# Kernel tuning notes

Measured on AMD Instinct MI355X. Metric: run time of the kernel, lower is better.

## Reference

```python
import jax, jax.numpy as jnp
import numpy as np

B = 65536
H = 50          # hidden_size
L = 6           # num_layers
IN = 3          # input_size
T = 3           # seq_len


def setup_inputs() -> dict:
    key = jax.random.key(0)
    ks = jax.random.split(key, 10)
    s = 0.1  # weight init scale
    return {
        "x":     jax.random.normal(ks[0], (B, IN, T), dtype=jnp.float32),
        "h0":    jax.random.normal(ks[1], (L, B, H), dtype=jnp.float32),
        "c0":    jax.random.normal(ks[2], (L, B, H), dtype=jnp.float32),
        "w_ih0": jax.random.normal(ks[3], (4 * H, IN), dtype=jnp.float32) * s,
        "w_ih":  jax.random.normal(ks[4], (L - 1, 4 * H, H), dtype=jnp.float32) * s,
        "w_hh":  jax.random.normal(ks[5], (L, 4 * H, H), dtype=jnp.float32) * s,
        "b_ih":  jax.random.normal(ks[6], (L, 4 * H), dtype=jnp.float32) * s,
        "b_hh":  jax.random.normal(ks[7], (L, 4 * H), dtype=jnp.float32) * s,
        "fc_w":  jax.random.normal(ks[8], (1, H), dtype=jnp.float32) * s,
        "fc_b":  jax.random.normal(ks[9], (1,), dtype=jnp.float32) * s,
    }


def _lstm_layer(x_seq, h, c, w_ih, w_hh, b):
    """x_seq: [T, B, in]; returns all hidden states [T, B, H].
    PyTorch gate order: i, f, g, o."""
    def step(carry, x_t):
        h, c = carry
        gates = x_t @ w_ih.T + h @ w_hh.T + b  # [B, 4H]
        i, f, g, o = jnp.split(gates, 4, axis=-1)
        i = jax.nn.sigmoid(i)
        f = jax.nn.sigmoid(f)
        g = jnp.tanh(g)
        o = jax.nn.sigmoid(o)
        c = f * c + i * g
        h = o * jnp.tanh(c)
        return (h, c), h

    _, ys = jax.lax.scan(step, (h, c), x_seq)
    return ys


def reference(x, h0, c0, w_ih0, w_ih, w_hh, b_ih, b_hh, fc_w, fc_b):
    # original forward: input.permute(0, 2, 1) -> [B, T, IN], batch_first LSTM
    seq = jnp.transpose(x, (2, 0, 1))  # [T, B, IN] (time-major for scan)
    b = b_ih + b_hh                    # combined bias per layer [L, 4H]
    ys = _lstm_layer(seq, h0[0], c0[0], w_ih0, w_hh[0], b[0])
    for l in range(1, L):
        ys = _lstm_layer(ys, h0[l], c0[l], w_ih[l - 1], w_hh[l], b[l])
    # dropout(0.2) is identity in eval mode; take last timestep then fc
    last = ys[-1]                      # [B, H]
    return last @ fc_w.T + fc_b        # [B, 1]
```

## Files before the change

### kernel.cpp

```cpp
#include <hip/hip_runtime.h>


namespace {

constexpr int H  = 50;
constexpr int L  = 6;
constexpr int T  = 3;
constexpr int IN = 3;
constexpr int M  = 64;
constexpr int BLK = 512;
constexpr int ROWS = 72;

using half8  = __attribute__((ext_vector_type(8))) _Float16;
using half2v = __attribute__((ext_vector_type(2))) _Float16;
using f32x4  = __attribute__((ext_vector_type(4))) float;

__device__ __forceinline__ float rcp_(float x) { return __builtin_amdgcn_rcpf(x); }
__device__ __forceinline__ float ex2(float x)  { return __builtin_amdgcn_exp2f(x); }

__global__ void wprep(const float* __restrict__ w_ih0, const float* __restrict__ w_ihL,
                      const float* __restrict__ w_hh,  const float* __restrict__ b_ih,
                      const float* __restrict__ b_hh,  _Float16* __restrict__ wbuf) {
  int t = blockIdx.x * 256 + threadIdx.x;
  if (t >= 384 * 64) return;
  int lam = t & 63, f = t >> 6;
  int nt = f & 15, s = (f >> 4) & 3, l = f >> 6;
  int n = nt * 16 + (lam & 15);
  int j = n >> 2, gate = n & 3, row = gate * 50 + j;
  float scale = (gate == 2) ? 2.8853900817779268f : 1.4426950408889634f;
  _Float16 o8[8];
#pragma unroll
  for (int jj = 0; jj < 8; ++jj) {
    int k = s * 32 + (lam >> 4) * 8 + jj;
    float v = 0.f;
    if (j < H) {
      if (s < 2) {
        int ksz = (l == 0) ? IN : H;
        if (k < ksz) v = (l == 0) ? w_ih0[row * IN + k]
                                  : w_ihL[((size_t)(l - 1) * 200 + row) * H + k];
      } else {
        int kh = k - 64;
        if (kh < H)        v = w_hh[((size_t)l * 200 + row) * H + kh];
        else if (kh == 63) v = b_ih[l * 200 + row] + b_hh[l * 200 + row];
      }
    }
    o8[jj] = (_Float16)(v * scale);
  }
  ((half8*)wbuf)[t] = *(half8*)o8;
}

__global__ __launch_bounds__(BLK, 4)
void lstm_mfma(const float* __restrict__ x,   const float* __restrict__ h0,
               const float* __restrict__ c0,  const float* __restrict__ fc_w,
               const float* __restrict__ fc_b, const _Float16* __restrict__ wbuf,
               float* __restrict__ out, int B) {
  const int tid = threadIdx.x;
  const int lam = tid & 63;
  const int q   = lam >> 4;
  const int lm  = lam & 15;
  const int bbase = blockIdx.x * M;
  const int ng  = __builtin_amdgcn_readfirstlane(tid >> 6);
  const int ntp = __builtin_amdgcn_readfirstlane((ng + blockIdx.x) & 7);
  const int ntg0 = 2 * ntp, ntg1 = 2 * ntp + 1;
  const bool live0 = (ntg0 <= 12);
  const bool live1 = (ntg1 <= 12);

  __shared__ __align__(16) _Float16 ys[2][T][M][ROWS];

  if (tid < T * M) {
    const int t = tid >> 6, m = tid & 63;
    const float* xs = x + (size_t)(bbase + m) * (IN * T) + t;
    _Float16* row = &ys[0][t][m][0];
    half2v p0; p0[0] = (_Float16)xs[0]; p0[1] = (_Float16)xs[3];
    half2v p1; p1[0] = (_Float16)xs[6]; p1[1] = (_Float16)0.f;
    *(half2v*)(row)     = p0;
    *(half2v*)(row + 2) = p1;
#pragma unroll
    for (int z = 0; z < 7; ++z)
      *(unsigned long long*)(row + 4 + 4 * z) = 0ull;
  }
  if (tid < 2 * T * M) {
    _Float16* row = &ys[0][0][0][0] + (size_t)tid * ROWS;
#pragma unroll
    for (int z = 0; z < 6; ++z)
      *(unsigned int*)(row + 50 + 2 * z) = 0u;
    half2v pb; pb[0] = (_Float16)0.f; pb[1] = (_Float16)1.f;
    *(half2v*)(row + 62) = pb;
  }
  __syncthreads();

  float cc[2][4];
  f32x4 xa[2][4];
  half8 W[2][4];
  const f32x4 z4 = {0.f, 0.f, 0.f, 0.f};

  for (int l = 0; l < L; ++l) {
    const int sb = l & 1, db = sb ^ 1;
    _Float16 (*src)[M][ROWS] = ys[sb];
    _Float16 (*dst)[M][ROWS] = ys[db];

#pragma unroll
    for (int nt = 0; nt < 2; ++nt) {
      const int ntg = nt ? ntg1 : ntg0;
      const bool lv = nt ? live1 : live0;
      const int j = 4 * ntg + q;
#pragma unroll
      for (int mt = 0; mt < 4; ++mt)
        cc[nt][mt] = (lv && j < H)
            ? c0[((size_t)l * B + bbase + mt * 16 + lm) * H + j] : 0.f;
    }
#pragma unroll
    for (int nt = 0; nt < 2; ++nt) {
      const int ntg = nt ? ntg1 : ntg0;
      const bool lv = nt ? live1 : live0;
      if (lv)
#pragma unroll
        for (int s = 0; s < 4; ++s)
          W[nt][s] = ((const half8*)wbuf)[((l * 4 + s) * 16 + ntg) * 64 + lam];
    }

    if (live0) {
#pragma unroll
      for (int s = 0; s < 2; ++s) {
        if (s == 1 && l == 0) continue;
        half8 Xf[4];
#pragma unroll
        for (int mt = 0; mt < 4; ++mt)
          Xf[mt] = *(const half8*)(&src[0][mt * 16 + lm][s * 32 + q * 8]);
#pragma unroll
        for (int mt = 0; mt < 4; ++mt)
          xa[0][mt] = __builtin_amdgcn_mfma_f32_16x16x32_f16(
              W[0][s], Xf[mt], s == 0 ? z4 : xa[0][mt], 0, 0, 0);
        if (live1)
#pragma unroll
          for (int mt = 0; mt < 4; ++mt)
            xa[1][mt] = __builtin_amdgcn_mfma_f32_16x16x32_f16(
                W[1][s], Xf[mt], s == 0 ? z4 : xa[1][mt], 0, 0, 0);
      }
    }

    {
      const int mg = tid >> 3, kpl = tid & 7;
      const float* hp = h0 + ((size_t)l * B + bbase + mg) * H + 2 * kpl;
      _Float16* dp = &dst[T - 1][mg][2 * kpl];
#pragma unroll
      for (int it = 0; it < 4; ++it) {
        if (it < 3 || kpl == 0) {
          float2 v = *(const float2*)(hp + 16 * it);
          half2v pv; pv[0] = (_Float16)v.x; pv[1] = (_Float16)v.y;
          *(half2v*)(dp + 16 * it) = pv;
        }
      }
    }
    __syncthreads();

#pragma unroll
    for (int t = 0; t < T; ++t) {
      const int hsl = (t == 0) ? T - 1 : t - 1;
      if (live0) {
#pragma unroll
        for (int s = 0; s < 2; ++s) {
          half8 Xf[4];
#pragma unroll
          for (int mt = 0; mt < 4; ++mt)
            Xf[mt] = *(const half8*)(&dst[hsl][mt * 16 + lm][s * 32 + q * 8]);
#pragma unroll
          for (int mt = 0; mt < 4; ++mt)
            xa[0][mt] = __builtin_amdgcn_mfma_f32_16x16x32_f16(
                W[0][s + 2], Xf[mt], xa[0][mt], 0, 0, 0);
          if (live1)
#pragma unroll
            for (int mt = 0; mt < 4; ++mt)
              xa[1][mt] = __builtin_amdgcn_mfma_f32_16x16x32_f16(
                  W[1][s + 2], Xf[mt], xa[1][mt], 0, 0, 0);
        }

#pragma unroll
        for (int nt = 0; nt < 2; ++nt) {
          if (nt && !live1) continue;
          const int ntg = nt ? ntg1 : ntg0;
          const int j = 4 * ntg + q;
#pragma unroll
          for (int mt = 0; mt < 4; ++mt) {
            const float ig = rcp_(1.f + ex2(-xa[nt][mt][0]));
            const float fg = rcp_(1.f + ex2(-xa[nt][mt][1]));
            const float gg = 2.f * rcp_(1.f + ex2(-xa[nt][mt][2])) - 1.f;
            const float og = rcp_(1.f + ex2(-xa[nt][mt][3]));
            const float cv = fg * cc[nt][mt] + ig * gg;
            cc[nt][mt] = cv;
            const float tc = 2.f * rcp_(1.f + ex2(-2.8853900817779268f * cv)) - 1.f;
            const float hv = og * tc;
            if (j < H)
              dst[t][mt * 16 + lm][j] = (_Float16)hv;
          }
        }

        if (t < T - 1) {
#pragma unroll
          for (int s = 0; s < 2; ++s) {
            if (s == 1 && l == 0) continue;
            half8 Xf[4];
#pragma unroll
            for (int mt = 0; mt < 4; ++mt)
              Xf[mt] = *(const half8*)(&src[t + 1][mt * 16 + lm][s * 32 + q * 8]);
#pragma unroll
            for (int mt = 0; mt < 4; ++mt)
              xa[0][mt] = __builtin_amdgcn_mfma_f32_16x16x32_f16(
                  W[0][s], Xf[mt], s == 0 ? z4 : xa[0][mt], 0, 0, 0);
            if (live1)
#pragma unroll
              for (int mt = 0; mt < 4; ++mt)
                xa[1][mt] = __builtin_amdgcn_mfma_f32_16x16x32_f16(
                    W[1][s], Xf[mt], s == 0 ? z4 : xa[1][mt], 0, 0, 0);
          }
        }
      }
      __syncthreads();
    }
  }

  {
    int m = tid >> 3, strip = tid & 7;
    float part = 0.f;
#pragma unroll
    for (int jj = 0; jj < 7; ++jj) {
      int j = strip + 8 * jj;
      if (j < H) part += fc_w[j] * (float)ys[0][T - 1][m][j];
    }
    part += __shfl_xor(part, 4);
    part += __shfl_xor(part, 2);
    part += __shfl_xor(part, 1);
    if (strip == 0) out[bbase + m] = part + fc_b[0];
  }
}

}

extern "C" void kernel_launch(void* const* d_in, const int* in_sizes, int n_in,
                              void* d_out, int out_size, void* d_ws, size_t ws_size,
                              hipStream_t stream) {
  const float* x     = (const float*)d_in[0];
  const float* h0    = (const float*)d_in[1];
  const float* c0    = (const float*)d_in[2];
  const float* w_ih0 = (const float*)d_in[3];
  const float* w_ih  = (const float*)d_in[4];
  const float* w_hh  = (const float*)d_in[5];
  const float* b_ih  = (const float*)d_in[6];
  const float* b_hh  = (const float*)d_in[7];
  const float* fc_w  = (const float*)d_in[8];
  const float* fc_b  = (const float*)d_in[9];
  float* out         = (float*)d_out;

  const int B = in_sizes[0] / (IN * T);
  _Float16* wbuf = (_Float16*)d_ws;

  wprep<<<(384 * 64 + 255) / 256, 256, 0, stream>>>(w_ih0, w_ih, w_hh, b_ih, b_hh, wbuf);
  lstm_mfma<<<B / M, BLK, 0, stream>>>(x, h0, c0, fc_w, fc_b, wbuf, out, B);
}
```

Measured before the change: 269.6 us.

## Software-pipeline LSTM timestep: interleave MFMA, gate activations and next-step input projection

Restructures the per-timestep loop so it walks the four row tiles one at a time. For each tile it issues the recurrent MFMAs, then runs the gate activations and the next timestep's input-projection MFMAs for the previous tile. LDS operand loads are double-buffered in 2-slot register arrays instead of 4-wide fragment arrays. The aim is to overlap transcendental VALU work and LDS latency with matrix-core work and to lower peak register use. The cost is more complex code whose real benefit depends on how the compiler schedules it.

```diff
diff --git a/kernel.cpp b/kernel.cpp
--- a/kernel.cpp
+++ b/kernel.cpp
@@ -154,69 +154,77 @@
     }
     __syncthreads();
 
+#define LD_H(s, mt) (*(const half8*)(&dst[hsl][(mt) * 16 + lm][(s) * 32 + q * 8]))
+#define LD_X(s, mt) (*(const half8*)(&src[t + 1][(mt) * 16 + lm][(s) * 32 + q * 8]))
+#define ACT1(nt, mt) do {                                                      \
+    const int j_ = 4 * ((nt) ? ntg1 : ntg0) + q;                               \
+    const float ig = rcp_(1.f + ex2(-xa[nt][mt][0]));                          \
+    const float fg = rcp_(1.f + ex2(-xa[nt][mt][1]));                          \
+    const float gg = 2.f * rcp_(1.f + ex2(-xa[nt][mt][2])) - 1.f;              \
+    const float og = rcp_(1.f + ex2(-xa[nt][mt][3]));                          \
+    const float cv = fg * cc[nt][mt] + ig * gg;                                \
+    cc[nt][mt] = cv;                                                           \
+    const float tc = 2.f * rcp_(1.f + ex2(-2.8853900817779268f * cv)) - 1.f;   \
+    const float hv = og * tc;                                                  \
+    if (j_ < H) dst[t][(mt) * 16 + lm][j_] = (_Float16)hv;                     \
+  } while (0)
+#define XM1(nt, mt) do {                                                       \
+    xa[nt][mt] = __builtin_amdgcn_mfma_f32_16x16x32_f16(                       \
+        W[nt][0], Xn[0][(mt) & 1], z4, 0, 0, 0);                               \
+    if (l > 0)                                                                 \
+      xa[nt][mt] = __builtin_amdgcn_mfma_f32_16x16x32_f16(                     \
+          W[nt][1], Xn[1][(mt) & 1], xa[nt][mt], 0, 0, 0);                     \
+  } while (0)
+#define STEP_TAIL(mt) do {                                                     \
+    ACT1(0, mt);                                                               \
+    if (live1) ACT1(1, mt);                                                    \
+    if (pre) { XM1(0, mt); if (live1) XM1(1, mt); }                            \
+  } while (0)
+
 #pragma unroll
     for (int t = 0; t < T; ++t) {
       const int hsl = (t == 0) ? T - 1 : t - 1;
       if (live0) {
-#pragma unroll
-        for (int s = 0; s < 2; ++s) {
-          half8 Xf[4];
-#pragma unroll
-          for (int mt = 0; mt < 4; ++mt)
-            Xf[mt] = *(const half8*)(&dst[hsl][mt * 16 + lm][s * 32 + q * 8]);
-#pragma unroll
-          for (int mt = 0; mt < 4; ++mt)
-            xa[0][mt] = __builtin_amdgcn_mfma_f32_16x16x32_f16(
-                W[0][s + 2], Xf[mt], xa[0][mt], 0, 0, 0);
-          if (live1)
-#pragma unroll
-            for (int mt = 0; mt < 4; ++mt)
-              xa[1][mt] = __builtin_amdgcn_mfma_f32_16x16x32_f16(
-                  W[1][s + 2], Xf[mt], xa[1][mt], 0, 0, 0);
+        const bool pre = (t < T - 1);
+        half8 Hf[2][2], Xn[2][2];
+        Hf[0][0] = LD_H(0, 0);
+        Hf[1][0] = LD_H(1, 0);
+        if (pre) {
+          Xn[0][0] = LD_X(0, 0);
+          if (l > 0) Xn[1][0] = LD_X(1, 0);
         }
-
-#pragma unroll
-        for (int nt = 0; nt < 2; ++nt) {
-          if (nt && !live1) continue;
-          const int ntg = nt ? ntg1 : ntg0;
-          const int j = 4 * ntg + q;
-#pragma unroll
-          for (int mt = 0; mt < 4; ++mt) {
-            const float ig = rcp_(1.f + ex2(-xa[nt][mt][0]));
-            const float fg = rcp_(1.f + ex2(-xa[nt][mt][1]));
-            const float gg = 2.f * rcp_(1.f + ex2(-xa[nt][mt][2])) - 1.f;
-            const float og = rcp_(1.f + ex2(-xa[nt][mt][3]));
-            const float cv = fg * cc[nt][mt] + ig * gg;
-            cc[nt][mt] = cv;
-            const float tc = 2.f * rcp_(1.f + ex2(-2.8853900817779268f * cv)) - 1.f;
-            const float hv = og * tc;
-            if (j < H)
-              dst[t][mt * 16 + lm][j] = (_Float16)hv;
+#pragma unroll
+        for (int mt = 0; mt < 4; ++mt) {
+          const int cur = mt & 1, nxt = cur ^ 1;
+          if (mt < 3) {
+            Hf[0][nxt] = LD_H(0, mt + 1);
+            Hf[1][nxt] = LD_H(1, mt + 1);
+          }
+          xa[0][mt] = __builtin_amdgcn_mfma_f32_16x16x32_f16(
+              W[0][2], Hf[0][cur], xa[0][mt], 0, 0, 0);
+          xa[0][mt] = __builtin_amdgcn_mfma_f32_16x16x32_f16(
+              W[0][3], Hf[1][cur], xa[0][mt], 0, 0, 0);
+          if (live1) {
+            xa[1][mt] = __builtin_amdgcn_mfma_f32_16x16x32_f16(
+                W[1][2], Hf[0][cur], xa[1][mt], 0, 0, 0);
+            xa[1][mt] = __builtin_amdgcn_mfma_f32_16x16x32_f16(
+                W[1][3], Hf[1][cur], xa[1][mt], 0, 0, 0);
+          }
+          if (mt > 0) STEP_TAIL(mt - 1);
+          if (mt < 3 && pre) {
+            Xn[0][nxt] = LD_X(0, mt + 1);
+            if (l > 0) Xn[1][nxt] = LD_X(1, mt + 1);
           }
         }
-
-        if (t < T - 1) {
-#pragma unroll
-          for (int s = 0; s < 2; ++s) {
-            if (s == 1 && l == 0) continue;
-            half8 Xf[4];
-#pragma unroll
-            for (int mt = 0; mt < 4; ++mt)
-              Xf[mt] = *(const half8*)(&src[t + 1][mt * 16 + lm][s * 32 + q * 8]);
-#pragma unroll
-            for (int mt = 0; mt < 4; ++mt)
-              xa[0][mt] = __builtin_amdgcn_mfma_f32_16x16x32_f16(
-                  W[0][s], Xf[mt], s == 0 ? z4 : xa[0][mt], 0, 0, 0);
-            if (live1)
-#pragma unroll
-              for (int mt = 0; mt < 4; ++mt)
-                xa[1][mt] = __builtin_amdgcn_mfma_f32_16x16x32_f16(
-                    W[1][s], Xf[mt], s == 0 ? z4 : xa[1][mt], 0, 0, 0);
-          }
-        }
+        STEP_TAIL(3);
       }
       __syncthreads();
     }
+#undef LD_H
+#undef LD_X
+#undef ACT1
+#undef XM1
+#undef STEP_TAIL
   }
 
   {
```

Result: no change. 271.6 us (+0.8%).

## Use 16 waves per block with one gate tile each and a rotating 5-slot LDS ring

Applied to the files above, without the earlier changes.

Doubles the block size from 8 to 16 waves so each wave owns a single 16-column gate tile instead of two, halving the per-wave MFMA and activation work and the register footprint. The layer double buffer of six timestep slots becomes a rotating ring of five slots, where each layer's outputs overwrite consumed inputs. This cuts LDS per block and lets more blocks fit per CU. The trade-off is that 3 of 16 waves are idle, and barriers now synchronise twice as many waves.

```diff
diff --git a/kernel.cpp b/kernel.cpp
--- a/kernel.cpp
+++ b/kernel.cpp
@@ -8,8 +8,9 @@
 constexpr int T  = 3;
 constexpr int IN = 3;
 constexpr int M  = 64;
-constexpr int BLK = 512;
+constexpr int BLK = 1024;
 constexpr int ROWS = 72;
+constexpr int NSLOT = 5;
 
 using half8  = __attribute__((ext_vector_type(8))) _Float16;
 using half2v = __attribute__((ext_vector_type(2))) _Float16;
@@ -49,7 +50,7 @@
   ((half8*)wbuf)[t] = *(half8*)o8;
 }
 
-__global__ __launch_bounds__(BLK, 4)
+__global__ __launch_bounds__(BLK, 8)
 void lstm_mfma(const float* __restrict__ x,   const float* __restrict__ h0,
                const float* __restrict__ c0,  const float* __restrict__ fc_w,
                const float* __restrict__ fc_b, const _Float16* __restrict__ wbuf,
@@ -59,18 +60,25 @@
   const int q   = lam >> 4;
   const int lm  = lam & 15;
   const int bbase = blockIdx.x * M;
-  const int ng  = __builtin_amdgcn_readfirstlane(tid >> 6);
-  const int ntp = __builtin_amdgcn_readfirstlane((ng + blockIdx.x) & 7);
-  const int ntg0 = 2 * ntp, ntg1 = 2 * ntp + 1;
-  const bool live0 = (ntg0 <= 12);
-  const bool live1 = (ntg1 <= 12);
-
-  __shared__ __align__(16) _Float16 ys[2][T][M][ROWS];
-
+  const int w   = __builtin_amdgcn_readfirstlane(tid >> 6);
+  const int ntg = __builtin_amdgcn_readfirstlane((w + blockIdx.x) & 15);
+  const bool live = (ntg <= 12);
+  const int j = 4 * ntg + q;
+
+  __shared__ __align__(16) _Float16 ys[NSLOT][M][ROWS];
+
+  if (tid < NSLOT * M) {
+    _Float16* row = &ys[0][0][0] + (size_t)tid * ROWS;
+#pragma unroll
+    for (int z = 0; z < 6; ++z)
+      *(unsigned int*)(row + 50 + 2 * z) = 0u;
+    half2v pb; pb[0] = (_Float16)0.f; pb[1] = (_Float16)1.f;
+    *(half2v*)(row + 62) = pb;
+  }
   if (tid < T * M) {
     const int t = tid >> 6, m = tid & 63;
     const float* xs = x + (size_t)(bbase + m) * (IN * T) + t;
-    _Float16* row = &ys[0][t][m][0];
+    _Float16* row = &ys[2 + t][m][0];
     half2v p0; p0[0] = (_Float16)xs[0]; p0[1] = (_Float16)xs[3];
     half2v p1; p1[0] = (_Float16)xs[6]; p1[1] = (_Float16)0.f;
     *(half2v*)(row)     = p0;
@@ -79,153 +87,109 @@
     for (int z = 0; z < 7; ++z)
       *(unsigned long long*)(row + 4 + 4 * z) = 0ull;
   }
-  if (tid < 2 * T * M) {
-    _Float16* row = &ys[0][0][0][0] + (size_t)tid * ROWS;
-#pragma unroll
-    for (int z = 0; z < 6; ++z)
-      *(unsigned int*)(row + 50 + 2 * z) = 0u;
-    half2v pb; pb[0] = (_Float16)0.f; pb[1] = (_Float16)1.f;
-    *(half2v*)(row + 62) = pb;
-  }
   __syncthreads();
 
-  float cc[2][4];
-  f32x4 xa[2][4];
-  half8 W[2][4];
+  float cc[4];
+  f32x4 xa[4];
+  half8 W4[4];
   const f32x4 z4 = {0.f, 0.f, 0.f, 0.f};
+  int b = 0;
 
   for (int l = 0; l < L; ++l) {
-    const int sb = l & 1, db = sb ^ 1;
-    _Float16 (*src)[M][ROWS] = ys[sb];
-    _Float16 (*dst)[M][ROWS] = ys[db];
-
-#pragma unroll
-    for (int nt = 0; nt < 2; ++nt) {
-      const int ntg = nt ? ntg1 : ntg0;
-      const bool lv = nt ? live1 : live0;
-      const int j = 4 * ntg + q;
+    const int sh0 = b;
+    int s1 = b + 1; if (s1 >= NSLOT) s1 -= NSLOT;
+    int s2 = b + 2; if (s2 >= NSLOT) s2 -= NSLOT;
+    int s3 = b + 3; if (s3 >= NSLOT) s3 -= NSLOT;
+    int s4 = b + 4; if (s4 >= NSLOT) s4 -= NSLOT;
+
+    if (live) {
 #pragma unroll
       for (int mt = 0; mt < 4; ++mt)
-        cc[nt][mt] = (lv && j < H)
+        cc[mt] = (j < H)
             ? c0[((size_t)l * B + bbase + mt * 16 + lm) * H + j] : 0.f;
-    }
-#pragma unroll
-    for (int nt = 0; nt < 2; ++nt) {
-      const int ntg = nt ? ntg1 : ntg0;
-      const bool lv = nt ? live1 : live0;
-      if (lv)
-#pragma unroll
-        for (int s = 0; s < 4; ++s)
-          W[nt][s] = ((const half8*)wbuf)[((l * 4 + s) * 16 + ntg) * 64 + lam];
-    }
-
-    if (live0) {
-#pragma unroll
-      for (int s = 0; s < 2; ++s) {
-        if (s == 1 && l == 0) continue;
-        half8 Xf[4];
-#pragma unroll
-        for (int mt = 0; mt < 4; ++mt)
-          Xf[mt] = *(const half8*)(&src[0][mt * 16 + lm][s * 32 + q * 8]);
-#pragma unroll
-        for (int mt = 0; mt < 4; ++mt)
-          xa[0][mt] = __builtin_amdgcn_mfma_f32_16x16x32_f16(
-              W[0][s], Xf[mt], s == 0 ? z4 : xa[0][mt], 0, 0, 0);
-        if (live1)
-#pragma unroll
-          for (int mt = 0; mt < 4; ++mt)
-            xa[1][mt] = __builtin_amdgcn_mfma_f32_16x16x32_f16(
-                W[1][s], Xf[mt], s == 0 ? z4 : xa[1][mt], 0, 0, 0);
-      }
-    }
-
+#pragma unroll
+      for (int s = 0; s < 4; ++s)
+        W4[s] = ((const half8*)wbuf)[((l * 4 + s) * 16 + ntg) * 64 + lam];
+#pragma unroll
+      for (int mt = 0; mt < 4; ++mt) {
+        half8 X0 = *(const half8*)(&ys[s2][mt * 16 + lm][q * 8]);
+        xa[mt] = __builtin_amdgcn_mfma_f32_16x16x32_f16(W4[0], X0, z4, 0, 0, 0);
+      }
+      if (l > 0) {
+#pragma unroll
+        for (int mt = 0; mt < 4; ++mt) {
+          half8 X1 = *(const half8*)(&ys[s2][mt * 16 + lm][32 + q * 8]);
+          xa[mt] = __builtin_amdgcn_mfma_f32_16x16x32_f16(W4[1], X1, xa[mt], 0, 0, 0);
+        }
+      }
+    }
     {
-      const int mg = tid >> 3, kpl = tid & 7;
+      const int mg = tid >> 4, kpl = tid & 15;
       const float* hp = h0 + ((size_t)l * B + bbase + mg) * H + 2 * kpl;
-      _Float16* dp = &dst[T - 1][mg][2 * kpl];
-#pragma unroll
-      for (int it = 0; it < 4; ++it) {
-        if (it < 3 || kpl == 0) {
-          float2 v = *(const float2*)(hp + 16 * it);
-          half2v pv; pv[0] = (_Float16)v.x; pv[1] = (_Float16)v.y;
-          *(half2v*)(dp + 16 * it) = pv;
+      _Float16* dp = &ys[sh0][mg][2 * kpl];
+      float2 v = *(const float2*)(hp);
+      half2v pv; pv[0] = (_Float16)v.x; pv[1] = (_Float16)v.y;
+      *(half2v*)dp = pv;
+      if (kpl < 9) {
+        float2 v2 = *(const float2*)(hp + 32);
+        half2v p2; p2[0] = (_Float16)v2.x; p2[1] = (_Float16)v2.y;
+        *(half2v*)(dp + 32) = p2;
+      }
+    }
+    __syncthreads();
+
+#pragma unroll
+    for (int t = 0; t < T; ++t) {
+      const int shs = (t == 0) ? sh0 : ((t == 1) ? s1 : s2);
+      const int sot = (t == 0) ? s1  : ((t == 1) ? s2 : s3);
+      const int sxt = (t == 0) ? s3  : s4;
+      if (live) {
+#pragma unroll
+        for (int s = 0; s < 2; ++s)
+#pragma unroll
+          for (int mt = 0; mt < 4; ++mt) {
+            half8 Hf = *(const half8*)(&ys[shs][mt * 16 + lm][s * 32 + q * 8]);
+            xa[mt] = __builtin_amdgcn_mfma_f32_16x16x32_f16(W4[2 + s], Hf, xa[mt], 0, 0, 0);
+          }
+#pragma unroll
+        for (int mt = 0; mt < 4; ++mt) {
+          const float ig = rcp_(1.f + ex2(-xa[mt][0]));
+          const float fg = rcp_(1.f + ex2(-xa[mt][1]));
+          const float gg = 2.f * rcp_(1.f + ex2(-xa[mt][2])) - 1.f;
+          const float og = rcp_(1.f + ex2(-xa[mt][3]));
+          const float cv = fg * cc[mt] + ig * gg;
+          cc[mt] = cv;
+          const float tc = 2.f * rcp_(1.f + ex2(-2.8853900817779268f * cv)) - 1.f;
+          if (j < H)
+            ys[sot][mt * 16 + lm][j] = (_Float16)(og * tc);
         }
-      }
-    }
-    __syncthreads();
-
-#pragma unroll
-    for (int t = 0; t < T; ++t) {
-      const int hsl = (t == 0) ? T - 1 : t - 1;
-      if (live0) {
-#pragma unroll
-        for (int s = 0; s < 2; ++s) {
-          half8 Xf[4];
-#pragma unroll
-          for (int mt = 0; mt < 4; ++mt)
-            Xf[mt] = *(const half8*)(&dst[hsl][mt * 16 + lm][s * 32 + q * 8]);
-#pragma unroll
-          for (int mt = 0; mt < 4; ++mt)
-            xa[0][mt] = __builtin_amdgcn_mfma_f32_16x16x32_f16(
-                W[0][s + 2], Xf[mt], xa[0][mt], 0, 0, 0);
-          if (live1)
-#pragma unroll
-            for (int mt = 0; mt < 4; ++mt)
-              xa[1][mt] = __builtin_amdgcn_mfma_f32_16x16x32_f16(
-                  W[1][s + 2], Xf[mt], xa[1][mt], 0, 0, 0);
-        }
-
-#pragma unroll
-        for (int nt = 0; nt < 2; ++nt) {
-          if (nt && !live1) continue;
-          const int ntg = nt ? ntg1 : ntg0;
-          const int j = 4 * ntg + q;
+        if (t < T - 1) {
 #pragma unroll
           for (int mt = 0; mt < 4; ++mt) {
-            const float ig = rcp_(1.f + ex2(-xa[nt][mt][0]));
-            const float fg = rcp_(1.f + ex2(-xa[nt][mt][1]));
-            const float gg = 2.f * rcp_(1.f + ex2(-xa[nt][mt][2])) - 1.f;
-            const float og = rcp_(1.f + ex2(-xa[nt][mt][3]));
-            const float cv = fg * cc[nt][mt] + ig * gg;
-            cc[nt][mt] = cv;
-            const float tc = 2.f * rcp_(1.f + ex2(-2.8853900817779268f * cv)) - 1.f;
-            const float hv = og * tc;
-            if (j < H)
-              dst[t][mt * 16 + lm][j] = (_Float16)hv;
+            half8 X0 = *(const half8*)(&ys[sxt][mt * 16 + lm][q * 8]);
+            xa[mt] = __builtin_amdgcn_mfma_f32_16x16x32_f16(W4[0], X0, z4, 0, 0, 0);
+          }
+          if (l > 0) {
+#pragma unroll
+            for (int mt = 0; mt < 4; ++mt) {
+              half8 X1 = *(const half8*)(&ys[sxt][mt * 16 + lm][32 + q * 8]);
+              xa[mt] = __builtin_amdgcn_mfma_f32_16x16x32_f16(W4[1], X1, xa[mt], 0, 0, 0);
+            }
           }
         }
-
-        if (t < T - 1) {
-#pragma unroll
-          for (int s = 0; s < 2; ++s) {
-            if (s == 1 && l == 0) continue;
-            half8 Xf[4];
-#pragma unroll
-            for (int mt = 0; mt < 4; ++mt)
-              Xf[mt] = *(const half8*)(&src[t + 1][mt * 16 + lm][s * 32 + q * 8]);
-#pragma unroll
-            for (int mt = 0; mt < 4; ++mt)
-              xa[0][mt] = __builtin_amdgcn_mfma_f32_16x16x32_f16(
-                  W[0][s], Xf[mt], s == 0 ? z4 : xa[0][mt], 0, 0, 0);
-            if (live1)
-#pragma unroll
-              for (int mt = 0; mt < 4; ++mt)
-                xa[1][mt] = __builtin_amdgcn_mfma_f32_16x16x32_f16(
-                    W[1][s], Xf[mt], s == 0 ? z4 : xa[1][mt], 0, 0, 0);
-          }
-        }
       }
       __syncthreads();
     }
-  }
-
-  {
+    b = (b == 0) ? (NSLOT - 1) : b - 1;
+  }
+
+  if (tid < 512) {
     int m = tid >> 3, strip = tid & 7;
     float part = 0.f;
 #pragma unroll
     for (int jj = 0; jj < 7; ++jj) {
-      int j = strip + 8 * jj;
-      if (j < H) part += fc_w[j] * (float)ys[0][T - 1][m][j];
+      int jf = strip + 8 * jj;
+      if (jf < H) part += fc_w[jf] * (float)ys[3][m][jf];
     }
     part += __shfl_xor(part, 4);
     part += __shfl_xor(part, 2);
```

Measured after the change: 268.1 us. About the same (-0.6%).

## Halve batch tile and use a five-slot rotating LDS ring for hidden states

Applied to the files above, without the earlier changes.

Halves the per-block batch tile from 64 to 32 rows and doubles the occupancy target in launch bounds to 8. Replaces the double-buffered [2][T] shared staging with a five-slot ring whose base index rotates each layer, so h0 and the outputs share slots and LDS use drops. The c0 and weight loads move inside the live-wave branch so idle waves skip them. Intent is more resident blocks per CU to hide latency, at the cost of reloading weights in twice as many blocks and more per-block overhead.

```diff
diff --git a/kernel.cpp b/kernel.cpp
--- a/kernel.cpp
+++ b/kernel.cpp
@@ -7,9 +7,10 @@
 constexpr int L  = 6;
 constexpr int T  = 3;
 constexpr int IN = 3;
-constexpr int M  = 64;
+constexpr int M  = 32;
 constexpr int BLK = 512;
 constexpr int ROWS = 72;
+constexpr int NSLOT = 5;
 
 using half8  = __attribute__((ext_vector_type(8))) _Float16;
 using half2v = __attribute__((ext_vector_type(2))) _Float16;
@@ -49,7 +50,7 @@
   ((half8*)wbuf)[t] = *(half8*)o8;
 }
 
-__global__ __launch_bounds__(BLK, 4)
+__global__ __launch_bounds__(BLK, 8)
 void lstm_mfma(const float* __restrict__ x,   const float* __restrict__ h0,
                const float* __restrict__ c0,  const float* __restrict__ fc_w,
                const float* __restrict__ fc_b, const _Float16* __restrict__ wbuf,
@@ -65,12 +66,20 @@
   const bool live0 = (ntg0 <= 12);
   const bool live1 = (ntg1 <= 12);
 
-  __shared__ __align__(16) _Float16 ys[2][T][M][ROWS];
-
+  __shared__ __align__(16) _Float16 ys[NSLOT][M][ROWS];
+
+  if (tid < NSLOT * M) {
+    _Float16* row = &ys[0][0][0] + (size_t)tid * ROWS;
+#pragma unroll
+    for (int z = 0; z < 6; ++z)
+      *(unsigned int*)(row + 50 + 2 * z) = 0u;
+    half2v pb; pb[0] = (_Float16)0.f; pb[1] = (_Float16)1.f;
+    *(half2v*)(row + 62) = pb;
+  }
   if (tid < T * M) {
-    const int t = tid >> 6, m = tid & 63;
+    const int t = tid >> 5, m = tid & 31;
     const float* xs = x + (size_t)(bbase + m) * (IN * T) + t;
-    _Float16* row = &ys[0][t][m][0];
+    _Float16* row = &ys[2 + t][m][0];
     half2v p0; p0[0] = (_Float16)xs[0]; p0[1] = (_Float16)xs[3];
     half2v p1; p1[0] = (_Float16)xs[6]; p1[1] = (_Float16)0.f;
     *(half2v*)(row)     = p0;
@@ -79,109 +88,103 @@
     for (int z = 0; z < 7; ++z)
       *(unsigned long long*)(row + 4 + 4 * z) = 0ull;
   }
-  if (tid < 2 * T * M) {
-    _Float16* row = &ys[0][0][0][0] + (size_t)tid * ROWS;
-#pragma unroll
-    for (int z = 0; z < 6; ++z)
-      *(unsigned int*)(row + 50 + 2 * z) = 0u;
-    half2v pb; pb[0] = (_Float16)0.f; pb[1] = (_Float16)1.f;
-    *(half2v*)(row + 62) = pb;
-  }
   __syncthreads();
 
-  float cc[2][4];
-  f32x4 xa[2][4];
+  float cc[2][2];
+  f32x4 xa[2][2];
   half8 W[2][4];
   const f32x4 z4 = {0.f, 0.f, 0.f, 0.f};
+  int b = 0;
 
   for (int l = 0; l < L; ++l) {
-    const int sb = l & 1, db = sb ^ 1;
-    _Float16 (*src)[M][ROWS] = ys[sb];
-    _Float16 (*dst)[M][ROWS] = ys[db];
-
-#pragma unroll
-    for (int nt = 0; nt < 2; ++nt) {
-      const int ntg = nt ? ntg1 : ntg0;
-      const bool lv = nt ? live1 : live0;
-      const int j = 4 * ntg + q;
-#pragma unroll
-      for (int mt = 0; mt < 4; ++mt)
-        cc[nt][mt] = (lv && j < H)
-            ? c0[((size_t)l * B + bbase + mt * 16 + lm) * H + j] : 0.f;
-    }
-#pragma unroll
-    for (int nt = 0; nt < 2; ++nt) {
-      const int ntg = nt ? ntg1 : ntg0;
-      const bool lv = nt ? live1 : live0;
-      if (lv)
-#pragma unroll
-        for (int s = 0; s < 4; ++s)
-          W[nt][s] = ((const half8*)wbuf)[((l * 4 + s) * 16 + ntg) * 64 + lam];
-    }
+    const int sh0 = b;
+    int s1 = b + 1; if (s1 >= NSLOT) s1 -= NSLOT;
+    int s2 = b + 2; if (s2 >= NSLOT) s2 -= NSLOT;
+    int s3 = b + 3; if (s3 >= NSLOT) s3 -= NSLOT;
+    int s4 = b + 4; if (s4 >= NSLOT) s4 -= NSLOT;
 
     if (live0) {
+#pragma unroll
+      for (int nt = 0; nt < 2; ++nt) {
+        const int ntg = nt ? ntg1 : ntg0;
+        const bool lv = nt ? live1 : live0;
+        const int j = 4 * ntg + q;
+#pragma unroll
+        for (int mt = 0; mt < 2; ++mt)
+          cc[nt][mt] = (lv && j < H)
+              ? c0[((size_t)l * B + bbase + mt * 16 + lm) * H + j] : 0.f;
+      }
+#pragma unroll
+      for (int nt = 0; nt < 2; ++nt) {
+        const int ntg = nt ? ntg1 : ntg0;
+        const bool lv = nt ? live1 : live0;
+        if (lv)
+#pragma unroll
+          for (int s = 0; s < 4; ++s)
+            W[nt][s] = ((const half8*)wbuf)[((l * 4 + s) * 16 + ntg) * 64 + lam];
+      }
 #pragma unroll
       for (int s = 0; s < 2; ++s) {
         if (s == 1 && l == 0) continue;
-        half8 Xf[4];
-#pragma unroll
-        for (int mt = 0; mt < 4; ++mt)
-          Xf[mt] = *(const half8*)(&src[0][mt * 16 + lm][s * 32 + q * 8]);
-#pragma unroll
-        for (int mt = 0; mt < 4; ++mt)
+        half8 Xf[2];
+#pragma unroll
+        for (int mt = 0; mt < 2; ++mt)
+          Xf[mt] = *(const half8*)(&ys[s2][mt * 16 + lm][s * 32 + q * 8]);
+#pragma unroll
+        for (int mt = 0; mt < 2; ++mt)
           xa[0][mt] = __builtin_amdgcn_mfma_f32_16x16x32_f16(
               W[0][s], Xf[mt], s == 0 ? z4 : xa[0][mt], 0, 0, 0);
         if (live1)
 #pragma unroll
-          for (int mt = 0; mt < 4; ++mt)
+          for (int mt = 0; mt < 2; ++mt)
             xa[1][mt] = __builtin_amdgcn_mfma_f32_16x16x32_f16(
                 W[1][s], Xf[mt], s == 0 ? z4 : xa[1][mt], 0, 0, 0);
       }
     }
-
     {
-      const int mg = tid >> 3, kpl = tid & 7;
+      const int mg = tid >> 4, kpl = tid & 15;
       const float* hp = h0 + ((size_t)l * B + bbase + mg) * H + 2 * kpl;
-      _Float16* dp = &dst[T - 1][mg][2 * kpl];
-#pragma unroll
-      for (int it = 0; it < 4; ++it) {
-        if (it < 3 || kpl == 0) {
-          float2 v = *(const float2*)(hp + 16 * it);
-          half2v pv; pv[0] = (_Float16)v.x; pv[1] = (_Float16)v.y;
-          *(half2v*)(dp + 16 * it) = pv;
+      _Float16* dp = &ys[sh0][mg][2 * kpl];
+      float2 v = *(const float2*)(hp);
+      half2v pv; pv[0] = (_Float16)v.x; pv[1] = (_Float16)v.y;
+      *(half2v*)dp = pv;
+      if (kpl < 9) {
+        float2 v2 = *(const float2*)(hp + 32);
+        half2v p2; p2[0] = (_Float16)v2.x; p2[1] = (_Float16)v2.y;
+        *(half2v*)(dp + 32) = p2;
+      }
+    }
+    __syncthreads();
+
+#pragma unroll
+    for (int t = 0; t < T; ++t) {
+      const int shs = (t == 0) ? sh0 : ((t == 1) ? s1 : s2);
+      const int sot = (t == 0) ? s1  : ((t == 1) ? s2 : s3);
+      const int sxt = (t == 0) ? s3  : s4;
+      if (live0) {
+#pragma unroll
+        for (int s = 0; s < 2; ++s) {
+          half8 Hf[2];
+#pragma unroll
+          for (int mt = 0; mt < 2; ++mt)
+            Hf[mt] = *(const half8*)(&ys[shs][mt * 16 + lm][s * 32 + q * 8]);
+#pragma unroll
+          for (int mt = 0; mt < 2; ++mt)
+            xa[0][mt] = __builtin_amdgcn_mfma_f32_16x16x32_f16(
+                W[0][2 + s], Hf[mt], xa[0][mt], 0, 0, 0);
+          if (live1)
+#pragma unroll
+            for (int mt = 0; mt < 2; ++mt)
+              xa[1][mt] = __builtin_amdgcn_mfma_f32_16x16x32_f16(
+                  W[1][2 + s], Hf[mt], xa[1][mt], 0, 0, 0);
         }
-      }
-    }
-    __syncthreads();
-
-#pragma unroll
-    for (int t = 0; t < T; ++t) {
-      const int hsl = (t == 0) ? T - 1 : t - 1;
-      if (live0) {
-#pragma unroll
-        for (int s = 0; s < 2; ++s) {
-          half8 Xf[4];
-#pragma unroll
-          for (int mt = 0; mt < 4; ++mt)
-            Xf[mt] = *(const half8*)(&dst[hsl][mt * 16 + lm][s * 32 + q * 8]);
-#pragma unroll
-          for (int mt = 0; mt < 4; ++mt)
-            xa[0][mt] = __builtin_amdgcn_mfma_f32_16x16x32_f16(
-                W[0][s + 2], Xf[mt], xa[0][mt], 0, 0, 0);
-          if (live1)
-#pragma unroll
-            for (int mt = 0; mt < 4; ++mt)
-              xa[1][mt] = __builtin_amdgcn_mfma_f32_16x16x32_f16(
-                  W[1][s + 2], Xf[mt], xa[1][mt], 0, 0, 0);
-        }
-
 #pragma unroll
         for (int nt = 0; nt < 2; ++nt) {
           if (nt && !live1) continue;
           const int ntg = nt ? ntg1 : ntg0;
           const int j = 4 * ntg + q;
 #pragma unroll
-          for (int mt = 0; mt < 4; ++mt) {
+          for (int mt = 0; mt < 2; ++mt) {
             const float ig = rcp_(1.f + ex2(-xa[nt][mt][0]));
             const float fg = rcp_(1.f + ex2(-xa[nt][mt][1]));
             const float gg = 2.f * rcp_(1.f + ex2(-xa[nt][mt][2])) - 1.f;
@@ -189,27 +192,25 @@
             const float cv = fg * cc[nt][mt] + ig * gg;
             cc[nt][mt] = cv;
             const float tc = 2.f * rcp_(1.f + ex2(-2.8853900817779268f * cv)) - 1.f;
-            const float hv = og * tc;
             if (j < H)
-              dst[t][mt * 16 + lm][j] = (_Float16)hv;
+              ys[sot][mt * 16 + lm][j] = (_Float16)(og * tc);
           }
         }
-
         if (t < T - 1) {
 #pragma unroll
           for (int s = 0; s < 2; ++s) {
             if (s == 1 && l == 0) continue;
-            half8 Xf[4];
-#pragma unroll
-            for (int mt = 0; mt < 4; ++mt)
-              Xf[mt] = *(const half8*)(&src[t + 1][mt * 16 + lm][s * 32 + q * 8]);
-#pragma unroll
-            for (int mt = 0; mt < 4; ++mt)
+            half8 Xf[2];
+#pragma unroll
+            for (int mt = 0; mt < 2; ++mt)
+              Xf[mt] = *(const half8*)(&ys[sxt][mt * 16 + lm][s * 32 + q * 8]);
+#pragma unroll
+            for (int mt = 0; mt < 2; ++mt)
               xa[0][mt] = __builtin_amdgcn_mfma_f32_16x16x32_f16(
                   W[0][s], Xf[mt], s == 0 ? z4 : xa[0][mt], 0, 0, 0);
             if (live1)
 #pragma unroll
-              for (int mt = 0; mt < 4; ++mt)
+              for (int mt = 0; mt < 2; ++mt)
                 xa[1][mt] = __builtin_amdgcn_mfma_f32_16x16x32_f16(
                     W[1][s], Xf[mt], s == 0 ? z4 : xa[1][mt], 0, 0, 0);
           }
@@ -217,15 +218,16 @@
       }
       __syncthreads();
     }
-  }
-
-  {
+    b = (b == 0) ? (NSLOT - 1) : b - 1;
+  }
+
+  if (tid < 8 * M) {
     int m = tid >> 3, strip = tid & 7;
     float part = 0.f;
 #pragma unroll
     for (int jj = 0; jj < 7; ++jj) {
-      int j = strip + 8 * jj;
-      if (j < H) part += fc_w[j] * (float)ys[0][T - 1][m][j];
+      int jf = strip + 8 * jj;
+      if (jf < H) part += fc_w[jf] * (float)ys[3][m][jf];
     }
     part += __shfl_xor(part, 4);
     part += __shfl_xor(part, 2);
```

Result: slower. 409.7 us (+52.0%).
